# Performance work log

Measured on AMD Instinct MI355X. Metric: run time of the kernel, lower is better.

## Reference

```python
import jax, jax.numpy as jnp
import numpy as np

N_ORDER = 64
PRED_LEN = 720
SEQ_LEN = 720
ENC_IN = 321
BATCH = 16


def _hippo_legs(N):
    # HiPPO-LegS continuous transition (A, B), float64 numpy
    q = np.arange(N, dtype=np.float64)
    col, row = np.meshgrid(q, q)
    r = 2.0 * q + 1.0
    M = -(np.where(row >= col, r, 0.0) - np.diag(q))
    T = np.sqrt(np.diag(2.0 * q + 1.0))
    A = T @ M @ np.linalg.inv(T)
    B = np.diag(T)[:, None].copy()
    return A, B


def _discretize_bilinear(A, B, dt):
    # scipy.signal.cont2discrete(..., method='bilinear') equivalent
    N = A.shape[0]
    I = np.eye(N)
    BL = np.linalg.inv(I - (dt / 2.0) * A)
    Ad = BL @ (I + (dt / 2.0) * A)
    Bd = (BL @ (dt * B)).squeeze(-1)
    return Ad, Bd


def _legendre_eval_matrix(N, dt):
    # ss.eval_legendre(np.arange(N)[:,None], 1 - 2*vals).T via 3-term recurrence
    vals = np.arange(0.0, 1.0, dt)
    x = 1.0 - 2.0 * vals
    Ps = [np.ones_like(x), x]
    for n in range(1, N - 1):
        Ps.append(((2.0 * n + 1.0) * x * Ps[-1] - n * Ps[-2]) / (n + 1.0))
    return np.stack(Ps[:N], axis=0).T  # [len(vals), N]


def setup_inputs() -> dict:
    key = jax.random.key(0)
    k1, k2, k3 = jax.random.split(key, 3)
    dt = 1.0 / PRED_LEN
    A, B = _hippo_legs(N_ORDER)
    Ad, Bd = _discretize_bilinear(A, B, dt)
    eval_matrix = _legendre_eval_matrix(N_ORDER, dt)
    bound = 1.0 / np.sqrt(N_ORDER)  # torch nn.Linear default init range
    return {
        "x_enc": jax.random.normal(k1, (BATCH, SEQ_LEN, ENC_IN), dtype=jnp.float32),
        "A": jnp.asarray(Ad, dtype=jnp.float32),
        "B_vec": jnp.asarray(Bd, dtype=jnp.float32),
        "eval_matrix": jnp.asarray(eval_matrix, dtype=jnp.float32),
        "W_mlp": jax.random.uniform(k2, (N_ORDER, N_ORDER), jnp.float32, -bound, bound),
        "b_mlp": jax.random.uniform(k3, (N_ORDER,), jnp.float32, -bound, bound),
        "affine_weight": jnp.ones((1, 1, ENC_IN), jnp.float32),
        "affine_bias": jnp.zeros((1, 1, ENC_IN), jnp.float32),
    }


def reference(x_enc, A, B_vec, eval_matrix, W_mlp, b_mlp, affine_weight, affine_bias):
    P, N = eval_matrix.shape  # pred_len, proj_degree

    # RevIN-style instance normalization (means/stdev detached in torch)
    means = jax.lax.stop_gradient(jnp.mean(x_enc, axis=1, keepdims=True))
    x = x_enc - means
    stdev = jax.lax.stop_gradient(jnp.sqrt(jnp.var(x, axis=1, keepdims=True) + 1e-5))
    x = x / stdev
    x = x * affine_weight + affine_bias

    x_in = x[:, -P:]                         # [B, P, E]
    xs = jnp.transpose(x_in, (1, 0, 2))      # [P, B, E]: time-major for scan
    c0 = jnp.zeros((x_in.shape[0], x_in.shape[2], N), x_enc.dtype)

    def step(c, f):
        # c_t = c_{t-1} @ A^T + f_t B  (HiPPO-LegS linear recurrence)
        c_new = c @ A.T + f[..., None] * B_vec
        return c_new, c_new

    _, cs = jax.lax.scan(step, c0, xs)       # [P, B, E, N]

    out1 = cs @ W_mlp.T + b_mlp              # mlp over coefficient dim N
    x_dec_c = out1[P - 1]                    # [B, E, N] (seq_len >= pred_len branch)
    x_dec = x_dec_c @ eval_matrix.T          # [B, E, P] Legendre reconstruction
    x_dec = jnp.transpose(x_dec, (0, 2, 1))  # [B, P, E]

    # de-normalize
    x_dec = (x_dec - affine_bias) / (affine_weight + 1e-10)
    x_dec = x_dec * stdev + means
    return x_dec
```

## Files before the change

### kernel.cpp

```cpp
#include <hip/hip_runtime.h>
#include <math.h>

#define BATCH 16
#define SEQ   720
#define ENC   321
#define NORD  64
#define PRED  720
#define NPAIR (BATCH*ENC)

#define WS_KT    0
#define WS_EWT   (WS_KT + PRED*NORD)
#define WS_EVB   (WS_EWT + NORD*PRED)
#define WS_A16   (WS_EVB + PRED)
#define WS_KSUMP (WS_A16 + 4096)
#define WS_G     (WS_KSUMP + 17*64)
#define WS_PSUM  (WS_G + 4*96*4096)
#define WS_PSS   (WS_PSUM + 4*16*6*64)

#define MV4(AR, SVP, OUTV) do {                                                   \
    float _a0=0.f,_a1=0.f,_a2=0.f,_a3=0.f;                                        \
    _Pragma("unroll")                                                             \
    for (int _k = 0; _k < 4; _k++) {                                              \
        float4 _v0 = *(const float4*)&(SVP)[16*_k];                               \
        float4 _v1 = *(const float4*)&(SVP)[16*_k+4];                             \
        float4 _v2 = *(const float4*)&(SVP)[16*_k+8];                             \
        float4 _v3 = *(const float4*)&(SVP)[16*_k+12];                            \
        _a0 += (AR)[16*_k+0]*_v0.x + (AR)[16*_k+1]*_v0.y                          \
             + (AR)[16*_k+2]*_v0.z + (AR)[16*_k+3]*_v0.w;                         \
        _a1 += (AR)[16*_k+4]*_v1.x + (AR)[16*_k+5]*_v1.y                          \
             + (AR)[16*_k+6]*_v1.z + (AR)[16*_k+7]*_v1.w;                         \
        _a2 += (AR)[16*_k+8]*_v2.x + (AR)[16*_k+9]*_v2.y                          \
             + (AR)[16*_k+10]*_v2.z + (AR)[16*_k+11]*_v2.w;                       \
        _a3 += (AR)[16*_k+12]*_v3.x + (AR)[16*_k+13]*_v3.y                        \
             + (AR)[16*_k+14]*_v3.z + (AR)[16*_k+15]*_v3.w;                       \
    }                                                                             \
    OUTV = (_a0+_a1)+(_a2+_a3);                                                   \
} while (0)

__global__ __launch_bounds__(256, 1) void prep(const float* __restrict__ A,
        const float* __restrict__ Bv, float* __restrict__ ws)
{
    __shared__ float sv[4][64];
    const int tid  = threadIdx.x;
    const int lane = tid & 63;
    const int wv   = tid >> 6;
    if (blockIdx.x < 16) {
        float ar[64];
        #pragma unroll
        for (int k = 0; k < 16; k++) {
            float4 v = *(const float4*)&A[lane*64 + 4*k];
            ar[4*k]=v.x; ar[4*k+1]=v.y; ar[4*k+2]=v.z; ar[4*k+3]=v.w;
        }
        const int j = blockIdx.x*4 + wv;
        sv[wv][lane] = (lane == j) ? 1.f : 0.f;
        for (int s = 0; s < 16; s++) {
            float nv;
            MV4(ar, &sv[wv][0], nv);
            sv[wv][lane] = nv;
        }
        ws[WS_A16 + lane*64 + j] = sv[wv][lane];
    } else {
        if (tid >= 64) return;
        float ar[64];
        #pragma unroll
        for (int k = 0; k < 16; k++) {
            float4 v = *(const float4*)&A[lane*64 + 4*k];
            ar[4*k]=v.x; ar[4*k+1]=v.y; ar[4*k+2]=v.z; ar[4*k+3]=v.w;
        }
        float* Kt = ws + WS_KT;
        float bv = Bv[lane];
        sv[0][lane] = bv;
        Kt[(size_t)719*64 + lane] = bv;
        float ksml = bv;
        for (int j = 1; j <= 15; j++) {
            float nv;
            MV4(ar, &sv[0][0], nv);
            sv[0][lane] = nv;
            Kt[(size_t)(719 - j)*64 + lane] = nv;
            ksml += nv;
        }
        ws[WS_KSUMP + 16*64 + lane] = ksml;
    }
}

__global__ __launch_bounds__(256, 1) void chainsEW(const float* __restrict__ evalm,
        const float* __restrict__ W, const float* __restrict__ bm,
        float* __restrict__ ws)
{
    __shared__ float dsm[64*61];
    const int tid  = threadIdx.x;
    const int lane = tid & 63;
    const int wv   = tid >> 6;
    if (blockIdx.x < 16) {
        if (tid >= 64) return;
        float* sv = dsm;
        const int r = blockIdx.x;
        const float* A16 = ws + WS_A16;
        float* Kt = ws + WS_KT;
        float ar16[64];
        #pragma unroll
        for (int k = 0; k < 16; k++) {
            float4 v = *(const float4*)&A16[lane*64 + 4*k];
            ar16[4*k]=v.x; ar16[4*k+1]=v.y; ar16[4*k+2]=v.z; ar16[4*k+3]=v.w;
        }
        float ksml = 0.f;
        sv[lane] = Kt[(size_t)(719 - r)*64 + lane];
        for (int j = r + 16; j <= 719; j += 16) {
            float nv;
            MV4(ar16, sv, nv);
            sv[lane] = nv;
            Kt[(size_t)(719 - j)*64 + lane] = nv;
            ksml += nv;
        }
        ws[WS_KSUMP + r*64 + lane] = ksml;
    } else {
        float* Et = dsm;
        const int r = blockIdx.x - 16;
        float wcol[64];
        #pragma unroll
        for (int n = 0; n < 64; n++) wcol[n] = W[n*64 + lane];
        float bv = bm[lane];
        #pragma unroll
        for (int k = 0; k < 15; k++) {
            int row = wv + k*4;
            int tp = r*60 + row;
            const float* ev = evalm + (size_t)tp*64;
            float a0=0.f,a1=0.f,a2=0.f,a3=0.f;
            #pragma unroll
            for (int kk = 0; kk < 4; kk++) {
                float4 e0_ = *(const float4*)&ev[16*kk];
                float4 e1_ = *(const float4*)&ev[16*kk+4];
                float4 e2_ = *(const float4*)&ev[16*kk+8];
                float4 e3_ = *(const float4*)&ev[16*kk+12];
                a0 += e0_.x*wcol[16*kk+0] + e0_.y*wcol[16*kk+1]
                    + e0_.z*wcol[16*kk+2] + e0_.w*wcol[16*kk+3];
                a1 += e1_.x*wcol[16*kk+4] + e1_.y*wcol[16*kk+5]
                    + e1_.z*wcol[16*kk+6] + e1_.w*wcol[16*kk+7];
                a2 += e2_.x*wcol[16*kk+8] + e2_.y*wcol[16*kk+9]
                    + e2_.z*wcol[16*kk+10] + e2_.w*wcol[16*kk+11];
                a3 += e3_.x*wcol[16*kk+12] + e3_.y*wcol[16*kk+13]
                    + e3_.z*wcol[16*kk+14] + e3_.w*wcol[16*kk+15];
            }
            Et[lane*61 + row] = (a0+a1)+(a2+a3);
            float pv = ev[lane] * bv;
            #pragma unroll
            for (int o = 32; o > 0; o >>= 1) pv += __shfl_down(pv, o);
            if (lane == 0) ws[WS_EVB + tp] = pv;
        }
        __syncthreads();
        for (int idx = tid; idx < 4096; idx += 256) {
            int m = idx >> 6, row = idx & 63;
            if (row < 60)
                ws[WS_EWT + (size_t)m*720 + r*60 + row] = Et[m*61 + row];
        }
    }
}

__device__ inline float4 ldx(const float* __restrict__ x, int b, int t, int e4)
{
    float4 r = make_float4(0.f,0.f,0.f,0.f);
    const float* p = x + ((size_t)b*SEQ + t)*ENC;
    if (e4 + 3 < ENC) r = *(const float4*)&p[e4];
    else {
        if (e4   < ENC) r.x = p[e4];
        if (e4+1 < ENC) r.y = p[e4+1];
        if (e4+2 < ENC) r.z = p[e4+2];
    }
    return r;
}

__global__ __launch_bounds__(256) void k2(const float* __restrict__ x,
        float* __restrict__ ws)
{
    __shared__ float xt[2][12*64];
    __shared__ float ks[2][12*64];
    __shared__ float redn[12*64];
    __shared__ float reds[12*64];
    const int tid = threadIdx.x;
    const int bid = blockIdx.x;
    const int b = bid / 24, rem = bid % 24;
    const int et = rem / 4, tsp = rem % 4;
    const int e0 = et*64, t0 = tsp*180;

    const bool xon = tid < 192;
    const bool kon = tid >= 64;
    const int sx_t  = tid >> 4;
    const int sx_e4 = (tid & 15) * 4;
    const int sk    = tid - 64;
    const int sk_t  = sk >> 4;
    const int sk_m4 = (sk & 15) * 4;

    const float* Kt = ws + WS_KT;
    float s0=0,s1=0,s2=0,s3=0, q0=0,q1=0,q2=0,q3=0;
    float4 rx = make_float4(0,0,0,0), rk = make_float4(0,0,0,0);

    if (xon) rx = ldx(x, b, t0 + sx_t, e0 + sx_e4);
    if (kon) rk = *(const float4*)&Kt[(size_t)(t0 + sk_t)*64 + sk_m4];
    if (xon) {
        *(float4*)&xt[0][sx_t*64 + sx_e4] = rx;
        s0+=rx.x; s1+=rx.y; s2+=rx.z; s3+=rx.w;
        q0+=rx.x*rx.x; q1+=rx.y*rx.y; q2+=rx.z*rx.z; q3+=rx.w*rx.w;
    }
    if (kon) *(float4*)&ks[0][sk_t*64 + sk_m4] = rk;

    const bool con = tid < 128;
    const int elg = tid & 7;
    const int mgr = tid >> 3;
    float acc[8][4];
    #pragma unroll
    for (int j = 0; j < 8; j++)
        #pragma unroll
        for (int i = 0; i < 4; i++) acc[j][i] = 0.f;

    for (int ch = 0; ch < 15; ch++) {
        if (ch + 1 < 15) {
            if (xon) rx = ldx(x, b, t0 + (ch+1)*12 + sx_t, e0 + sx_e4);
            if (kon) rk = *(const float4*)&Kt[(size_t)(t0 + (ch+1)*12 + sk_t)*64 + sk_m4];
        }
        __syncthreads();
        const float* xb = xt[ch & 1];
        const float* kb = ks[ch & 1];
        if (con) {
            #pragma unroll
            for (int tt = 0; tt < 12; tt++) {
                float4 fa = *(const float4*)&xb[tt*64 + elg*8];
                float4 fb = *(const float4*)&xb[tt*64 + elg*8 + 4];
                float4 kv = *(const float4*)&kb[tt*64 + mgr*4];
                acc[0][0]+=fa.x*kv.x; acc[0][1]+=fa.x*kv.y; acc[0][2]+=fa.x*kv.z; acc[0][3]+=fa.x*kv.w;
                acc[1][0]+=fa.y*kv.x; acc[1][1]+=fa.y*kv.y; acc[1][2]+=fa.y*kv.z; acc[1][3]+=fa.y*kv.w;
                acc[2][0]+=fa.z*kv.x; acc[2][1]+=fa.z*kv.y; acc[2][2]+=fa.z*kv.z; acc[2][3]+=fa.z*kv.w;
                acc[3][0]+=fa.w*kv.x; acc[3][1]+=fa.w*kv.y; acc[3][2]+=fa.w*kv.z; acc[3][3]+=fa.w*kv.w;
                acc[4][0]+=fb.x*kv.x; acc[4][1]+=fb.x*kv.y; acc[4][2]+=fb.x*kv.z; acc[4][3]+=fb.x*kv.w;
                acc[5][0]+=fb.y*kv.x; acc[5][1]+=fb.y*kv.y; acc[5][2]+=fb.y*kv.z; acc[5][3]+=fb.y*kv.w;
                acc[6][0]+=fb.z*kv.x; acc[6][1]+=fb.z*kv.y; acc[6][2]+=fb.z*kv.z; acc[6][3]+=fb.z*kv.w;
                acc[7][0]+=fb.w*kv.x; acc[7][1]+=fb.w*kv.y; acc[7][2]+=fb.w*kv.z; acc[7][3]+=fb.w*kv.w;
            }
        }
        if (ch + 1 < 15) {
            if (xon) {
                *(float4*)&xt[(ch+1)&1][sx_t*64 + sx_e4] = rx;
                s0+=rx.x; s1+=rx.y; s2+=rx.z; s3+=rx.w;
                q0+=rx.x*rx.x; q1+=rx.y*rx.y; q2+=rx.z*rx.z; q3+=rx.w*rx.w;
            }
            if (kon) *(float4*)&ks[(ch+1)&1][sk_t*64 + sk_m4] = rk;
        }
    }

    if (con) {
        float* g = ws + WS_G + (size_t)(tsp*96 + b*6 + et)*4096;
        #pragma unroll
        for (int i = 0; i < 4; i++) {
            float* gr = g + (mgr*4 + i)*64 + elg*8;
            *(float4*)&gr[0] = make_float4(acc[0][i], acc[1][i], acc[2][i], acc[3][i]);
            *(float4*)&gr[4] = make_float4(acc[4][i], acc[5][i], acc[6][i], acc[7][i]);
        }
    }

    __syncthreads();
    if (xon) {
        redn[sx_t*64 + sx_e4+0] = s0; redn[sx_t*64 + sx_e4+1] = s1;
        redn[sx_t*64 + sx_e4+2] = s2; redn[sx_t*64 + sx_e4+3] = s3;
        reds[sx_t*64 + sx_e4+0] = q0; reds[sx_t*64 + sx_e4+1] = q1;
        reds[sx_t*64 + sx_e4+2] = q2; reds[sx_t*64 + sx_e4+3] = q3;
    }
    __syncthreads();
    if (tid < 64) {
        float s = 0.f, q = 0.f;
        #pragma unroll
        for (int rr = 0; rr < 12; rr++) { s += redn[rr*64 + tid]; q += reds[rr*64 + tid]; }
        const size_t o = (size_t)((tsp*16 + b)*6 + et)*64 + tid;
        ws[WS_PSUM + o] = s;
        ws[WS_PSS  + o] = q;
    }
}

__global__ __launch_bounds__(256) void k3f(const float* __restrict__ aw,
        const float* __restrict__ ab, const float* __restrict__ ws,
        float* __restrict__ out)
{
    __shared__ float Cm[64*132];
    __shared__ float EWm[64*68];
    __shared__ float ssc[128], ssh[128], smean[128], ssd[128], siaw[128], sabe[128];
    __shared__ float kss[64];
    const int tid = threadIdx.x;
    const int b   = blockIdx.x / 12;
    const int rr  = blockIdx.x % 12;
    const int eT  = rr / 4;
    const int tq  = rr % 4;
    const int e0  = eT * 128;
    const int et0 = eT * 2;

    if (tid < 128) {
        const int el = tid, e = e0 + el;
        const int et = et0 + (el >> 6), eli = el & 63;
        float s = 0.f, q = 0.f;
        #pragma unroll
        for (int tsp = 0; tsp < 4; tsp++) {
            const size_t o = (size_t)((tsp*16 + b)*6 + et)*64 + eli;
            s += ws[WS_PSUM + o];
            q += ws[WS_PSS  + o];
        }
        float mean = s * (1.0f/SEQ);
        float var  = q * (1.0f/SEQ) - mean*mean;
        float sd   = sqrtf(var + 1e-5f);
        if (e < ENC) {
            float a = aw[e], av = ab[e];
            float sc = a / sd;
            ssc[el] = sc; ssh[el] = av - mean*sc;
            smean[el] = mean; ssd[el] = sd;
            siaw[el] = 1.0f/(a + 1e-10f); sabe[el] = av;
        } else {
            ssc[el]=0.f; ssh[el]=0.f; smean[el]=0.f; ssd[el]=0.f; siaw[el]=0.f; sabe[el]=0.f;
        }
    }
    if (tid < 64) {
        float s = 0.f;
        #pragma unroll
        for (int p = 0; p < 17; p++) s += ws[WS_KSUMP + p*64 + tid];
        kss[tid] = s;
    }
    __syncthreads();

    const float* G = ws + WS_G;
    #pragma unroll
    for (int k = 0; k < 8; k++) {
        int slot = k*256 + tid;
        int m = slot >> 5, el4 = (slot & 31) * 4;
        int et = et0 + (el4 >> 6), eli4 = el4 & 63;
        size_t base = (size_t)(b*6 + et)*4096 + m*64 + eli4;
        float4 g0 = *(const float4*)&G[base];
        float4 g1 = *(const float4*)&G[base + (size_t) 96*4096];
        float4 g2 = *(const float4*)&G[base + (size_t)192*4096];
        float4 g3 = *(const float4*)&G[base + (size_t)288*4096];
        float km = kss[m];
        float4 sc = *(const float4*)&ssc[el4];
        float4 sh = *(const float4*)&ssh[el4];
        float4 c;
        c.x = sc.x*(g0.x+g1.x+g2.x+g3.x) + sh.x*km;
        c.y = sc.y*(g0.y+g1.y+g2.y+g3.y) + sh.y*km;
        c.z = sc.z*(g0.z+g1.z+g2.z+g3.z) + sh.z*km;
        c.w = sc.w*(g0.w+g1.w+g2.w+g3.w) + sh.w*km;
        *(float4*)&Cm[m*132 + el4] = c;
    }
    __syncthreads();

    const float* EWT = ws + WS_EWT;
    const float* evb = ws + WS_EVB;
    const int tx = tid & 31;
    const int ty = tid >> 5;

    const int elb = tx*4;
    const int ebase = e0 + elb;
    float4 sab  = *(const float4*)&sabe[elb];
    float4 sia  = *(const float4*)&siaw[elb];
    float4 ssd4 = *(const float4*)&ssd[elb];
    float4 smn  = *(const float4*)&smean[elb];

    for (int ti = 0; ti < 3; ti++) {
        const int tt0 = (tq*3 + ti) * 64;
        if (ti > 0) __syncthreads();
        #pragma unroll
        for (int k = 0; k < 4; k++) {
            int slot = k*256 + tid;
            int m = slot >> 4, t4 = (slot & 15)*4;
            int tp = tt0 + t4;
            float4 v;
            if (tp + 3 < PRED) v = *(const float4*)&EWT[(size_t)m*720 + tp];
            else {
                v = make_float4(0.f,0.f,0.f,0.f);
                if (tp   < PRED) v.x = EWT[(size_t)m*720 + tp];
                if (tp+1 < PRED) v.y = EWT[(size_t)m*720 + tp+1];
                if (tp+2 < PRED) v.z = EWT[(size_t)m*720 + tp+2];
            }
            *(float4*)&EWm[m*68 + t4] = v;
        }
        __syncthreads();

        float acc[8][4];
        #pragma unroll
        for (int i = 0; i < 8; i++)
            #pragma unroll
            for (int j = 0; j < 4; j++) acc[i][j] = 0.f;

        #pragma unroll 4
        for (int m = 0; m < 64; m++) {
            float4 c4 = *(const float4*)&Cm[m*132 + tx*4];
            float4 w0 = *(const float4*)&EWm[m*68 + ty*8];
            float4 w1 = *(const float4*)&EWm[m*68 + ty*8 + 4];
            acc[0][0]+=w0.x*c4.x; acc[0][1]+=w0.x*c4.y; acc[0][2]+=w0.x*c4.z; acc[0][3]+=w0.x*c4.w;
            acc[1][0]+=w0.y*c4.x; acc[1][1]+=w0.y*c4.y; acc[1][2]+=w0.y*c4.z; acc[1][3]+=w0.y*c4.w;
            acc[2][0]+=w0.z*c4.x; acc[2][1]+=w0.z*c4.y; acc[2][2]+=w0.z*c4.z; acc[2][3]+=w0.z*c4.w;
            acc[3][0]+=w0.w*c4.x; acc[3][1]+=w0.w*c4.y; acc[3][2]+=w0.w*c4.z; acc[3][3]+=w0.w*c4.w;
            acc[4][0]+=w1.x*c4.x; acc[4][1]+=w1.x*c4.y; acc[4][2]+=w1.x*c4.z; acc[4][3]+=w1.x*c4.w;
            acc[5][0]+=w1.y*c4.x; acc[5][1]+=w1.y*c4.y; acc[5][2]+=w1.y*c4.z; acc[5][3]+=w1.y*c4.w;
            acc[6][0]+=w1.z*c4.x; acc[6][1]+=w1.z*c4.y; acc[6][2]+=w1.z*c4.z; acc[6][3]+=w1.z*c4.w;
            acc[7][0]+=w1.w*c4.x; acc[7][1]+=w1.w*c4.y; acc[7][2]+=w1.w*c4.z; acc[7][3]+=w1.w*c4.w;
        }

        #pragma unroll
        for (int i = 0; i < 8; i++) {
            int tp = tt0 + ty*8 + i;
            if (tp < PRED) {
                float ev = evb[tp];
                float* op = out + ((size_t)b*PRED + tp)*ENC;
                if (ebase + 3 < ENC) {
                    float4 o;
                    o.x = (acc[i][0] + ev - sab.x) * sia.x * ssd4.x + smn.x;
                    o.y = (acc[i][1] + ev - sab.y) * sia.y * ssd4.y + smn.y;
                    o.z = (acc[i][2] + ev - sab.z) * sia.z * ssd4.z + smn.z;
                    o.w = (acc[i][3] + ev - sab.w) * sia.w * ssd4.w + smn.w;
                    *(float4*)&op[ebase] = o;
                } else {
                    if (ebase   < ENC) op[ebase  ] = (acc[i][0]+ev-sab.x)*sia.x*ssd4.x+smn.x;
                    if (ebase+1 < ENC) op[ebase+1] = (acc[i][1]+ev-sab.y)*sia.y*ssd4.y+smn.y;
                    if (ebase+2 < ENC) op[ebase+2] = (acc[i][2]+ev-sab.z)*sia.z*ssd4.z+smn.z;
                }
            }
        }
    }
}

extern "C" void kernel_launch(void* const* d_in, const int* in_sizes, int n_in,
                              void* d_out, int out_size, void* d_ws, size_t ws_size,
                              hipStream_t stream)
{
    const float* x     = (const float*)d_in[0];
    const float* A     = (const float*)d_in[1];
    const float* Bv    = (const float*)d_in[2];
    const float* evalm = (const float*)d_in[3];
    const float* W     = (const float*)d_in[4];
    const float* bm    = (const float*)d_in[5];
    const float* aw    = (const float*)d_in[6];
    const float* ab    = (const float*)d_in[7];
    float* ws  = (float*)d_ws;
    float* out = (float*)d_out;

    prep    <<<17, 256, 0, stream>>>(A, Bv, ws);
    chainsEW<<<28, 256, 0, stream>>>(evalm, W, bm, ws);
    k2      <<<BATCH*6*4, 256, 0, stream>>>(x, ws);
    k3f     <<<192, 256, 0, stream>>>(aw, ab, ws, out);
}
```

Measured before the change: 151.4 us.

## Restructure k2 as register-direct slab reduction and retile k3f output GEMM

k2 drops its shared-memory double-buffered tiles and has each thread stream x and the kernel rows straight from global memory into register accumulators. The time axis is split into 8 slabs instead of 4, doubling the grid. k3f now loads the whole 192-step EW tile once and computes a 12x8 register tile per thread, and the denormalisation is folded into a single multiply-add. The changes aim for more parallelism and fewer barriers, at the cost of more partial sums to reduce and more uncoalesced-like strided x loads.

```diff
diff --git a/kernel.cpp b/kernel.cpp
--- a/kernel.cpp
+++ b/kernel.cpp
@@ -6,7 +6,9 @@
 #define ENC   321
 #define NORD  64
 #define PRED  720
-#define NPAIR (BATCH*ENC)
+
+#define NSLAB 8
+#define TSLAB 90
 
 #define WS_KT    0
 #define WS_EWT   (WS_KT + PRED*NORD)
@@ -14,8 +16,8 @@
 #define WS_A16   (WS_EVB + PRED)
 #define WS_KSUMP (WS_A16 + 4096)
 #define WS_G     (WS_KSUMP + 17*64)
-#define WS_PSUM  (WS_G + 4*96*4096)
-#define WS_PSS   (WS_PSUM + 4*16*6*64)
+#define WS_PSUM  (WS_G + NSLAB*96*4096)
+#define WS_PSS   (WS_PSUM + NSLAB*16*6*64)
 
 #define MV4(AR, SVP, OUTV) do {                                                   \
     float _a0=0.f,_a1=0.f,_a2=0.f,_a3=0.f;                                        \
@@ -156,137 +158,81 @@
     }
 }
 
-__device__ inline float4 ldx(const float* __restrict__ x, int b, int t, int e4)
-{
-    float4 r = make_float4(0.f,0.f,0.f,0.f);
-    const float* p = x + ((size_t)b*SEQ + t)*ENC;
-    if (e4 + 3 < ENC) r = *(const float4*)&p[e4];
-    else {
-        if (e4   < ENC) r.x = p[e4];
-        if (e4+1 < ENC) r.y = p[e4+1];
-        if (e4+2 < ENC) r.z = p[e4+2];
-    }
-    return r;
-}
-
 __global__ __launch_bounds__(256) void k2(const float* __restrict__ x,
         float* __restrict__ ws)
 {
-    __shared__ float xt[2][12*64];
-    __shared__ float ks[2][12*64];
-    __shared__ float redn[12*64];
-    __shared__ float reds[12*64];
     const int tid = threadIdx.x;
     const int bid = blockIdx.x;
-    const int b = bid / 24, rem = bid % 24;
-    const int et = rem / 4, tsp = rem % 4;
-    const int e0 = et*64, t0 = tsp*180;
-
-    const bool xon = tid < 192;
-    const bool kon = tid >= 64;
-    const int sx_t  = tid >> 4;
-    const int sx_e4 = (tid & 15) * 4;
-    const int sk    = tid - 64;
-    const int sk_t  = sk >> 4;
-    const int sk_m4 = (sk & 15) * 4;
-
-    const float* Kt = ws + WS_KT;
-    float s0=0,s1=0,s2=0,s3=0, q0=0,q1=0,q2=0,q3=0;
-    float4 rx = make_float4(0,0,0,0), rk = make_float4(0,0,0,0);
-
-    if (xon) rx = ldx(x, b, t0 + sx_t, e0 + sx_e4);
-    if (kon) rk = *(const float4*)&Kt[(size_t)(t0 + sk_t)*64 + sk_m4];
-    if (xon) {
-        *(float4*)&xt[0][sx_t*64 + sx_e4] = rx;
-        s0+=rx.x; s1+=rx.y; s2+=rx.z; s3+=rx.w;
-        q0+=rx.x*rx.x; q1+=rx.y*rx.y; q2+=rx.z*rx.z; q3+=rx.w*rx.w;
-    }
-    if (kon) *(float4*)&ks[0][sk_t*64 + sk_m4] = rk;
-
-    const bool con = tid < 128;
-    const int elg = tid & 7;
-    const int mgr = tid >> 3;
-    float acc[8][4];
-    #pragma unroll
-    for (int j = 0; j < 8; j++)
-        #pragma unroll
-        for (int i = 0; i < 4; i++) acc[j][i] = 0.f;
-
-    for (int ch = 0; ch < 15; ch++) {
-        if (ch + 1 < 15) {
-            if (xon) rx = ldx(x, b, t0 + (ch+1)*12 + sx_t, e0 + sx_e4);
-            if (kon) rk = *(const float4*)&Kt[(size_t)(t0 + (ch+1)*12 + sk_t)*64 + sk_m4];
-        }
-        __syncthreads();
-        const float* xb = xt[ch & 1];
-        const float* kb = ks[ch & 1];
-        if (con) {
-            #pragma unroll
-            for (int tt = 0; tt < 12; tt++) {
-                float4 fa = *(const float4*)&xb[tt*64 + elg*8];
-                float4 fb = *(const float4*)&xb[tt*64 + elg*8 + 4];
-                float4 kv = *(const float4*)&kb[tt*64 + mgr*4];
-                acc[0][0]+=fa.x*kv.x; acc[0][1]+=fa.x*kv.y; acc[0][2]+=fa.x*kv.z; acc[0][3]+=fa.x*kv.w;
-                acc[1][0]+=fa.y*kv.x; acc[1][1]+=fa.y*kv.y; acc[1][2]+=fa.y*kv.z; acc[1][3]+=fa.y*kv.w;
-                acc[2][0]+=fa.z*kv.x; acc[2][1]+=fa.z*kv.y; acc[2][2]+=fa.z*kv.z; acc[2][3]+=fa.z*kv.w;
-                acc[3][0]+=fa.w*kv.x; acc[3][1]+=fa.w*kv.y; acc[3][2]+=fa.w*kv.z; acc[3][3]+=fa.w*kv.w;
-                acc[4][0]+=fb.x*kv.x; acc[4][1]+=fb.x*kv.y; acc[4][2]+=fb.x*kv.z; acc[4][3]+=fb.x*kv.w;
-                acc[5][0]+=fb.y*kv.x; acc[5][1]+=fb.y*kv.y; acc[5][2]+=fb.y*kv.z; acc[5][3]+=fb.y*kv.w;
-                acc[6][0]+=fb.z*kv.x; acc[6][1]+=fb.z*kv.y; acc[6][2]+=fb.z*kv.z; acc[6][3]+=fb.z*kv.w;
-                acc[7][0]+=fb.w*kv.x; acc[7][1]+=fb.w*kv.y; acc[7][2]+=fb.w*kv.z; acc[7][3]+=fb.w*kv.w;
-            }
-        }
-        if (ch + 1 < 15) {
-            if (xon) {
-                *(float4*)&xt[(ch+1)&1][sx_t*64 + sx_e4] = rx;
-                s0+=rx.x; s1+=rx.y; s2+=rx.z; s3+=rx.w;
-                q0+=rx.x*rx.x; q1+=rx.y*rx.y; q2+=rx.z*rx.z; q3+=rx.w*rx.w;
-            }
-            if (kon) *(float4*)&ks[(ch+1)&1][sk_t*64 + sk_m4] = rk;
-        }
-    }
-
-    if (con) {
-        float* g = ws + WS_G + (size_t)(tsp*96 + b*6 + et)*4096;
-        #pragma unroll
-        for (int i = 0; i < 4; i++) {
-            float* gr = g + (mgr*4 + i)*64 + elg*8;
-            *(float4*)&gr[0] = make_float4(acc[0][i], acc[1][i], acc[2][i], acc[3][i]);
-            *(float4*)&gr[4] = make_float4(acc[4][i], acc[5][i], acc[6][i], acc[7][i]);
-        }
-    }
-
-    __syncthreads();
-    if (xon) {
-        redn[sx_t*64 + sx_e4+0] = s0; redn[sx_t*64 + sx_e4+1] = s1;
-        redn[sx_t*64 + sx_e4+2] = s2; redn[sx_t*64 + sx_e4+3] = s3;
-        reds[sx_t*64 + sx_e4+0] = q0; reds[sx_t*64 + sx_e4+1] = q1;
-        reds[sx_t*64 + sx_e4+2] = q2; reds[sx_t*64 + sx_e4+3] = q3;
-    }
-    __syncthreads();
-    if (tid < 64) {
-        float s = 0.f, q = 0.f;
-        #pragma unroll
-        for (int rr = 0; rr < 12; rr++) { s += redn[rr*64 + tid]; q += reds[rr*64 + tid]; }
-        const size_t o = (size_t)((tsp*16 + b)*6 + et)*64 + tid;
-        ws[WS_PSUM + o] = s;
-        ws[WS_PSS  + o] = q;
-    }
-}
+    const int b = bid / 48, rem = bid % 48;
+    const int et = rem >> 3, tsp = rem & 7;
+    const int e0 = et*64, t0 = tsp*TSLAB;
+
+    const int lane = tid & 63;
+    const int wv   = tid >> 6;
+    const int eg   = lane & 7;
+    const int mg   = lane >> 3;
+    const int el   = wv*16 + eg*2;
+    const int e    = e0 + el;
+
+    const float* xp = x + ((size_t)b*SEQ + t0)*ENC + e;
+    const float* kp = ws + WS_KT + (size_t)t0*64 + mg*8;
+
+    float a0[8], a1[8];
+    #pragma unroll
+    for (int i = 0; i < 8; i++) { a0[i]=0.f; a1[i]=0.f; }
+    float s0=0.f, s1=0.f, q0=0.f, q1=0.f;
+    const bool v1 = (e + 1 < ENC);
+    const bool v0 = (e < ENC);
+
+    #pragma unroll 6
+    for (int t = 0; t < TSLAB; t++) {
+        float xa = 0.f, xb = 0.f;
+        if (v1)      { float2 xv = *(const float2*)xp; xa = xv.x; xb = xv.y; }
+        else if (v0) { xa = *xp; }
+        float4 k0 = *(const float4*)kp;
+        float4 k1 = *(const float4*)(kp + 4);
+        a0[0]+=k0.x*xa; a1[0]+=k0.x*xb;
+        a0[1]+=k0.y*xa; a1[1]+=k0.y*xb;
+        a0[2]+=k0.z*xa; a1[2]+=k0.z*xb;
+        a0[3]+=k0.w*xa; a1[3]+=k0.w*xb;
+        a0[4]+=k1.x*xa; a1[4]+=k1.x*xb;
+        a0[5]+=k1.y*xa; a1[5]+=k1.y*xb;
+        a0[6]+=k1.z*xa; a1[6]+=k1.z*xb;
+        a0[7]+=k1.w*xa; a1[7]+=k1.w*xb;
+        s0 += xa; q0 += xa*xa;
+        s1 += xb; q1 += xb*xb;
+        xp += ENC; kp += 64;
+    }
+
+    float* g = ws + WS_G + (size_t)(tsp*96 + b*6 + et)*4096 + el;
+    #pragma unroll
+    for (int i = 0; i < 8; i++)
+        *(float2*)&g[(mg*8 + i)*64] = make_float2(a0[i], a1[i]);
+
+    if (mg == 0) {
+        const size_t o = (size_t)((tsp*16 + b)*6 + et)*64 + el;
+        *(float2*)&ws[WS_PSUM + o] = make_float2(s0, s1);
+        *(float2*)&ws[WS_PSS  + o] = make_float2(q0, q1);
+    }
+}
+
+#define K3ROW(r, wvv) \
+    acc[r][0]+=(wvv)*c0.x; acc[r][1]+=(wvv)*c0.y; acc[r][2]+=(wvv)*c0.z; acc[r][3]+=(wvv)*c0.w; \
+    acc[r][4]+=(wvv)*c1.x; acc[r][5]+=(wvv)*c1.y; acc[r][6]+=(wvv)*c1.z; acc[r][7]+=(wvv)*c1.w;
 
 __global__ __launch_bounds__(256) void k3f(const float* __restrict__ aw,
         const float* __restrict__ ab, const float* __restrict__ ws,
         float* __restrict__ out)
 {
-    __shared__ float Cm[64*132];
-    __shared__ float EWm[64*68];
-    __shared__ float ssc[128], ssh[128], smean[128], ssd[128], siaw[128], sabe[128];
+    __shared__ float Cm[64*192];
+    __shared__ float EWm[64*196];
+    __shared__ float ssc[128], ssh[128], sP[128], sQ[128];
     __shared__ float kss[64];
     const int tid = threadIdx.x;
     const int b   = blockIdx.x / 12;
     const int rr  = blockIdx.x % 12;
-    const int eT  = rr / 4;
-    const int tq  = rr % 4;
+    const int eT  = rr >> 2;
+    const int tq  = rr & 3;
     const int e0  = eT * 128;
     const int et0 = eT * 2;
 
@@ -295,7 +241,7 @@
         const int et = et0 + (el >> 6), eli = el & 63;
         float s = 0.f, q = 0.f;
         #pragma unroll
-        for (int tsp = 0; tsp < 4; tsp++) {
+        for (int tsp = 0; tsp < NSLAB; tsp++) {
             const size_t o = (size_t)((tsp*16 + b)*6 + et)*64 + eli;
             s += ws[WS_PSUM + o];
             q += ws[WS_PSS  + o];
@@ -306,11 +252,11 @@
         if (e < ENC) {
             float a = aw[e], av = ab[e];
             float sc = a / sd;
+            float P  = sd / (a + 1e-10f);
             ssc[el] = sc; ssh[el] = av - mean*sc;
-            smean[el] = mean; ssd[el] = sd;
-            siaw[el] = 1.0f/(a + 1e-10f); sabe[el] = av;
+            sP[el]  = P;  sQ[el]  = mean - av*P;
         } else {
-            ssc[el]=0.f; ssh[el]=0.f; smean[el]=0.f; ssd[el]=0.f; siaw[el]=0.f; sabe[el]=0.f;
+            ssc[el]=0.f; ssh[el]=0.f; sP[el]=0.f; sQ[el]=0.f;
         }
     }
     if (tid < 64) {
@@ -328,93 +274,97 @@
         int m = slot >> 5, el4 = (slot & 31) * 4;
         int et = et0 + (el4 >> 6), eli4 = el4 & 63;
         size_t base = (size_t)(b*6 + et)*4096 + m*64 + eli4;
-        float4 g0 = *(const float4*)&G[base];
-        float4 g1 = *(const float4*)&G[base + (size_t) 96*4096];
-        float4 g2 = *(const float4*)&G[base + (size_t)192*4096];
-        float4 g3 = *(const float4*)&G[base + (size_t)288*4096];
+        float4 gs = make_float4(0.f,0.f,0.f,0.f);
+        #pragma unroll
+        for (int s2 = 0; s2 < NSLAB; s2++) {
+            float4 gv = *(const float4*)&G[base + (size_t)s2*96*4096];
+            gs.x += gv.x; gs.y += gv.y; gs.z += gv.z; gs.w += gv.w;
+        }
         float km = kss[m];
         float4 sc = *(const float4*)&ssc[el4];
         float4 sh = *(const float4*)&ssh[el4];
         float4 c;
-        c.x = sc.x*(g0.x+g1.x+g2.x+g3.x) + sh.x*km;
-        c.y = sc.y*(g0.y+g1.y+g2.y+g3.y) + sh.y*km;
-        c.z = sc.z*(g0.z+g1.z+g2.z+g3.z) + sh.z*km;
-        c.w = sc.w*(g0.w+g1.w+g2.w+g3.w) + sh.w*km;
-        *(float4*)&Cm[m*132 + el4] = c;
+        c.x = sc.x*gs.x + sh.x*km;
+        c.y = sc.y*gs.y + sh.y*km;
+        c.z = sc.z*gs.z + sh.z*km;
+        c.w = sc.w*gs.w + sh.w*km;
+        *(float4*)&Cm[m*192 + (el4>>3)*12 + (el4&7)] = c;
+    }
+
+    const float* EWT = ws + WS_EWT;
+    #pragma unroll
+    for (int it = 0; it < 12; it++) {
+        int slot = it*256 + tid;
+        int m = slot / 48, t4 = (slot % 48) * 4;
+        int tp = tq*192 + t4;
+        float4 v;
+        if (tp + 3 < PRED) v = *(const float4*)&EWT[(size_t)m*720 + tp];
+        else {
+            v = make_float4(0.f,0.f,0.f,0.f);
+            if (tp   < PRED) v.x = EWT[(size_t)m*720 + tp];
+            if (tp+1 < PRED) v.y = EWT[(size_t)m*720 + tp+1];
+            if (tp+2 < PRED) v.z = EWT[(size_t)m*720 + tp+2];
+        }
+        *(float4*)&EWm[m*196 + t4] = v;
     }
     __syncthreads();
 
-    const float* EWT = ws + WS_EWT;
+    const int tx = tid & 15;
+    const int ty = tid >> 4;
+    float acc[12][8];
+    #pragma unroll
+    for (int r = 0; r < 12; r++)
+        #pragma unroll
+        for (int j = 0; j < 8; j++) acc[r][j] = 0.f;
+
+    const float* cb = Cm  + tx*12;
+    const float* wb = EWm + ty*12;
+    #pragma unroll 2
+    for (int m = 0; m < 64; m++) {
+        float4 c0 = *(const float4*)&cb[m*192];
+        float4 c1 = *(const float4*)&cb[m*192 + 4];
+        float4 w0 = *(const float4*)&wb[m*196];
+        float4 w1 = *(const float4*)&wb[m*196 + 4];
+        float4 w2 = *(const float4*)&wb[m*196 + 8];
+        K3ROW(0,  w0.x) K3ROW(1,  w0.y) K3ROW(2,  w0.z) K3ROW(3,  w0.w)
+        K3ROW(4,  w1.x) K3ROW(5,  w1.y) K3ROW(6,  w1.z) K3ROW(7,  w1.w)
+        K3ROW(8,  w2.x) K3ROW(9,  w2.y) K3ROW(10, w2.z) K3ROW(11, w2.w)
+    }
+
+    const int elb = tx*8;
+    const int eb  = e0 + elb;
+    float4 Pa = *(const float4*)&sP[elb];
+    float4 Pb = *(const float4*)&sP[elb+4];
+    float4 Qa = *(const float4*)&sQ[elb];
+    float4 Qb = *(const float4*)&sQ[elb+4];
     const float* evb = ws + WS_EVB;
-    const int tx = tid & 31;
-    const int ty = tid >> 5;
-
-    const int elb = tx*4;
-    const int ebase = e0 + elb;
-    float4 sab  = *(const float4*)&sabe[elb];
-    float4 sia  = *(const float4*)&siaw[elb];
-    float4 ssd4 = *(const float4*)&ssd[elb];
-    float4 smn  = *(const float4*)&smean[elb];
-
-    for (int ti = 0; ti < 3; ti++) {
-        const int tt0 = (tq*3 + ti) * 64;
-        if (ti > 0) __syncthreads();
-        #pragma unroll
-        for (int k = 0; k < 4; k++) {
-            int slot = k*256 + tid;
-            int m = slot >> 4, t4 = (slot & 15)*4;
-            int tp = tt0 + t4;
-            float4 v;
-            if (tp + 3 < PRED) v = *(const float4*)&EWT[(size_t)m*720 + tp];
-            else {
-                v = make_float4(0.f,0.f,0.f,0.f);
-                if (tp   < PRED) v.x = EWT[(size_t)m*720 + tp];
-                if (tp+1 < PRED) v.y = EWT[(size_t)m*720 + tp+1];
-                if (tp+2 < PRED) v.z = EWT[(size_t)m*720 + tp+2];
-            }
-            *(float4*)&EWm[m*68 + t4] = v;
-        }
-        __syncthreads();
-
-        float acc[8][4];
-        #pragma unroll
-        for (int i = 0; i < 8; i++)
-            #pragma unroll
-            for (int j = 0; j < 4; j++) acc[i][j] = 0.f;
-
-        #pragma unroll 4
-        for (int m = 0; m < 64; m++) {
-            float4 c4 = *(const float4*)&Cm[m*132 + tx*4];
-            float4 w0 = *(const float4*)&EWm[m*68 + ty*8];
-            float4 w1 = *(const float4*)&EWm[m*68 + ty*8 + 4];
-            acc[0][0]+=w0.x*c4.x; acc[0][1]+=w0.x*c4.y; acc[0][2]+=w0.x*c4.z; acc[0][3]+=w0.x*c4.w;
-            acc[1][0]+=w0.y*c4.x; acc[1][1]+=w0.y*c4.y; acc[1][2]+=w0.y*c4.z; acc[1][3]+=w0.y*c4.w;
-            acc[2][0]+=w0.z*c4.x; acc[2][1]+=w0.z*c4.y; acc[2][2]+=w0.z*c4.z; acc[2][3]+=w0.z*c4.w;
-            acc[3][0]+=w0.w*c4.x; acc[3][1]+=w0.w*c4.y; acc[3][2]+=w0.w*c4.z; acc[3][3]+=w0.w*c4.w;
-            acc[4][0]+=w1.x*c4.x; acc[4][1]+=w1.x*c4.y; acc[4][2]+=w1.x*c4.z; acc[4][3]+=w1.x*c4.w;
-            acc[5][0]+=w1.y*c4.x; acc[5][1]+=w1.y*c4.y; acc[5][2]+=w1.y*c4.z; acc[5][3]+=w1.y*c4.w;
-            acc[6][0]+=w1.z*c4.x; acc[6][1]+=w1.z*c4.y; acc[6][2]+=w1.z*c4.z; acc[6][3]+=w1.z*c4.w;
-            acc[7][0]+=w1.w*c4.x; acc[7][1]+=w1.w*c4.y; acc[7][2]+=w1.w*c4.z; acc[7][3]+=w1.w*c4.w;
-        }
-
-        #pragma unroll
-        for (int i = 0; i < 8; i++) {
-            int tp = tt0 + ty*8 + i;
-            if (tp < PRED) {
-                float ev = evb[tp];
-                float* op = out + ((size_t)b*PRED + tp)*ENC;
-                if (ebase + 3 < ENC) {
-                    float4 o;
-                    o.x = (acc[i][0] + ev - sab.x) * sia.x * ssd4.x + smn.x;
-                    o.y = (acc[i][1] + ev - sab.y) * sia.y * ssd4.y + smn.y;
-                    o.z = (acc[i][2] + ev - sab.z) * sia.z * ssd4.z + smn.z;
-                    o.w = (acc[i][3] + ev - sab.w) * sia.w * ssd4.w + smn.w;
-                    *(float4*)&op[ebase] = o;
-                } else {
-                    if (ebase   < ENC) op[ebase  ] = (acc[i][0]+ev-sab.x)*sia.x*ssd4.x+smn.x;
-                    if (ebase+1 < ENC) op[ebase+1] = (acc[i][1]+ev-sab.y)*sia.y*ssd4.y+smn.y;
-                    if (ebase+2 < ENC) op[ebase+2] = (acc[i][2]+ev-sab.z)*sia.z*ssd4.z+smn.z;
-                }
+    #pragma unroll
+    for (int r = 0; r < 12; r++) {
+        int tp = tq*192 + ty*12 + r;
+        if (tp < PRED) {
+            float ev = evb[tp];
+            float* op = out + ((size_t)b*PRED + tp)*ENC;
+            if (eb + 7 < ENC) {
+                float4 o0, o1;
+                o0.x = (acc[r][0]+ev)*Pa.x + Qa.x;
+                o0.y = (acc[r][1]+ev)*Pa.y + Qa.y;
+                o0.z = (acc[r][2]+ev)*Pa.z + Qa.z;
+                o0.w = (acc[r][3]+ev)*Pa.w + Qa.w;
+                o1.x = (acc[r][4]+ev)*Pb.x + Qb.x;
+                o1.y = (acc[r][5]+ev)*Pb.y + Qb.y;
+                o1.z = (acc[r][6]+ev)*Pb.z + Qb.z;
+                o1.w = (acc[r][7]+ev)*Pb.w + Qb.w;
+                *(float4*)&op[eb]   = o0;
+                *(float4*)&op[eb+4] = o1;
+            } else {
+                if (eb   < ENC) op[eb  ] = (acc[r][0]+ev)*Pa.x + Qa.x;
+                if (eb+1 < ENC) op[eb+1] = (acc[r][1]+ev)*Pa.y + Qa.y;
+                if (eb+2 < ENC) op[eb+2] = (acc[r][2]+ev)*Pa.z + Qa.z;
+                if (eb+3 < ENC) op[eb+3] = (acc[r][3]+ev)*Pa.w + Qa.w;
+                if (eb+4 < ENC) op[eb+4] = (acc[r][4]+ev)*Pb.x + Qb.x;
+                if (eb+5 < ENC) op[eb+5] = (acc[r][5]+ev)*Pb.y + Qb.y;
+                if (eb+6 < ENC) op[eb+6] = (acc[r][6]+ev)*Pb.z + Qb.z;
+                if (eb+7 < ENC) op[eb+7] = (acc[r][7]+ev)*Pb.w + Qb.w;
             }
         }
     }
@@ -437,6 +387,6 @@
 
     prep    <<<17, 256, 0, stream>>>(A, Bv, ws);
     chainsEW<<<28, 256, 0, stream>>>(evalm, W, bm, ws);
-    k2      <<<BATCH*6*4, 256, 0, stream>>>(x, ws);
+    k2      <<<16*6*NSLAB, 256, 0, stream>>>(x, ws);
     k3f     <<<192, 256, 0, stream>>>(aw, ab, ws, out);
 }
```

Measured after the change: 157.5 us. +4.0%, slower.

## Enlarge k3f register tile to 12x8 and load full EW slice once

Applied to the files above, without the earlier changes.

The output-projection kernel now loads its whole 192-step slice of the evaluation weights into shared memory once, instead of three 64-step passes each with its own barrier. Each thread computes a 12x8 register tile instead of 8x4, which raises FMA-to-LDS ratio, and the C tile uses a padded 12-stride layout. The de-normalization is folded into one multiply-add per element. In exchange it uses more shared memory (about 100KB) and more registers, which may reduce occupancy.

```diff
diff --git a/kernel.cpp b/kernel.cpp
--- a/kernel.cpp
+++ b/kernel.cpp
@@ -274,19 +274,23 @@
     }
 }
 
+#define K3ROW(r, wvv) \
+    acc[r][0]+=(wvv)*c0.x; acc[r][1]+=(wvv)*c0.y; acc[r][2]+=(wvv)*c0.z; acc[r][3]+=(wvv)*c0.w; \
+    acc[r][4]+=(wvv)*c1.x; acc[r][5]+=(wvv)*c1.y; acc[r][6]+=(wvv)*c1.z; acc[r][7]+=(wvv)*c1.w;
+
 __global__ __launch_bounds__(256) void k3f(const float* __restrict__ aw,
         const float* __restrict__ ab, const float* __restrict__ ws,
         float* __restrict__ out)
 {
-    __shared__ float Cm[64*132];
-    __shared__ float EWm[64*68];
-    __shared__ float ssc[128], ssh[128], smean[128], ssd[128], siaw[128], sabe[128];
+    __shared__ float Cm[64*192];
+    __shared__ float EWm[64*196];
+    __shared__ float ssc[128], ssh[128], sP[128], sQ[128];
     __shared__ float kss[64];
     const int tid = threadIdx.x;
     const int b   = blockIdx.x / 12;
     const int rr  = blockIdx.x % 12;
-    const int eT  = rr / 4;
-    const int tq  = rr % 4;
+    const int eT  = rr >> 2;
+    const int tq  = rr & 3;
     const int e0  = eT * 128;
     const int et0 = eT * 2;
 
@@ -306,11 +310,11 @@
         if (e < ENC) {
             float a = aw[e], av = ab[e];
             float sc = a / sd;
+            float P  = sd / (a + 1e-10f);
             ssc[el] = sc; ssh[el] = av - mean*sc;
-            smean[el] = mean; ssd[el] = sd;
-            siaw[el] = 1.0f/(a + 1e-10f); sabe[el] = av;
+            sP[el]  = P;  sQ[el]  = mean - av*P;
         } else {
-            ssc[el]=0.f; ssh[el]=0.f; smean[el]=0.f; ssd[el]=0.f; siaw[el]=0.f; sabe[el]=0.f;
+            ssc[el]=0.f; ssh[el]=0.f; sP[el]=0.f; sQ[el]=0.f;
         }
     }
     if (tid < 64) {
@@ -340,81 +344,83 @@
         c.y = sc.y*(g0.y+g1.y+g2.y+g3.y) + sh.y*km;
         c.z = sc.z*(g0.z+g1.z+g2.z+g3.z) + sh.z*km;
         c.w = sc.w*(g0.w+g1.w+g2.w+g3.w) + sh.w*km;
-        *(float4*)&Cm[m*132 + el4] = c;
+        *(float4*)&Cm[m*192 + (el4>>3)*12 + (el4&7)] = c;
+    }
+
+    const float* EWT = ws + WS_EWT;
+    #pragma unroll
+    for (int it = 0; it < 12; it++) {
+        int slot = it*256 + tid;
+        int m = slot / 48, t4 = (slot % 48) * 4;
+        int tp = tq*192 + t4;
+        float4 v;
+        if (tp + 3 < PRED) v = *(const float4*)&EWT[(size_t)m*720 + tp];
+        else {
+            v = make_float4(0.f,0.f,0.f,0.f);
+            if (tp   < PRED) v.x = EWT[(size_t)m*720 + tp];
+            if (tp+1 < PRED) v.y = EWT[(size_t)m*720 + tp+1];
+            if (tp+2 < PRED) v.z = EWT[(size_t)m*720 + tp+2];
+        }
+        *(float4*)&EWm[m*196 + t4] = v;
     }
     __syncthreads();
 
-    const float* EWT = ws + WS_EWT;
+    const int tx = tid & 15;
+    const int ty = tid >> 4;
+    float acc[12][8];
+    #pragma unroll
+    for (int r = 0; r < 12; r++)
+        #pragma unroll
+        for (int j = 0; j < 8; j++) acc[r][j] = 0.f;
+
+    const float* cb = Cm  + tx*12;
+    const float* wb = EWm + ty*12;
+    #pragma unroll 2
+    for (int m = 0; m < 64; m++) {
+        float4 c0 = *(const float4*)&cb[m*192];
+        float4 c1 = *(const float4*)&cb[m*192 + 4];
+        float4 w0 = *(const float4*)&wb[m*196];
+        float4 w1 = *(const float4*)&wb[m*196 + 4];
+        float4 w2 = *(const float4*)&wb[m*196 + 8];
+        K3ROW(0,  w0.x) K3ROW(1,  w0.y) K3ROW(2,  w0.z) K3ROW(3,  w0.w)
+        K3ROW(4,  w1.x) K3ROW(5,  w1.y) K3ROW(6,  w1.z) K3ROW(7,  w1.w)
+        K3ROW(8,  w2.x) K3ROW(9,  w2.y) K3ROW(10, w2.z) K3ROW(11, w2.w)
+    }
+
+    const int elb = tx*8;
+    const int eb  = e0 + elb;
+    float4 Pa = *(const float4*)&sP[elb];
+    float4 Pb = *(const float4*)&sP[elb+4];
+    float4 Qa = *(const float4*)&sQ[elb];
+    float4 Qb = *(const float4*)&sQ[elb+4];
     const float* evb = ws + WS_EVB;
-    const int tx = tid & 31;
-    const int ty = tid >> 5;
-
-    const int elb = tx*4;
-    const int ebase = e0 + elb;
-    float4 sab  = *(const float4*)&sabe[elb];
-    float4 sia  = *(const float4*)&siaw[elb];
-    float4 ssd4 = *(const float4*)&ssd[elb];
-    float4 smn  = *(const float4*)&smean[elb];
-
-    for (int ti = 0; ti < 3; ti++) {
-        const int tt0 = (tq*3 + ti) * 64;
-        if (ti > 0) __syncthreads();
-        #pragma unroll
-        for (int k = 0; k < 4; k++) {
-            int slot = k*256 + tid;
-            int m = slot >> 4, t4 = (slot & 15)*4;
-            int tp = tt0 + t4;
-            float4 v;
-            if (tp + 3 < PRED) v = *(const float4*)&EWT[(size_t)m*720 + tp];
-            else {
-                v = make_float4(0.f,0.f,0.f,0.f);
-                if (tp   < PRED) v.x = EWT[(size_t)m*720 + tp];
-                if (tp+1 < PRED) v.y = EWT[(size_t)m*720 + tp+1];
-                if (tp+2 < PRED) v.z = EWT[(size_t)m*720 + tp+2];
-            }
-            *(float4*)&EWm[m*68 + t4] = v;
-        }
-        __syncthreads();
-
-        float acc[8][4];
-        #pragma unroll
-        for (int i = 0; i < 8; i++)
-            #pragma unroll
-            for (int j = 0; j < 4; j++) acc[i][j] = 0.f;
-
-        #pragma unroll 4
-        for (int m = 0; m < 64; m++) {
-            float4 c4 = *(const float4*)&Cm[m*132 + tx*4];
-            float4 w0 = *(const float4*)&EWm[m*68 + ty*8];
-            float4 w1 = *(const float4*)&EWm[m*68 + ty*8 + 4];
-            acc[0][0]+=w0.x*c4.x; acc[0][1]+=w0.x*c4.y; acc[0][2]+=w0.x*c4.z; acc[0][3]+=w0.x*c4.w;
-            acc[1][0]+=w0.y*c4.x; acc[1][1]+=w0.y*c4.y; acc[1][2]+=w0.y*c4.z; acc[1][3]+=w0.y*c4.w;
-            acc[2][0]+=w0.z*c4.x; acc[2][1]+=w0.z*c4.y; acc[2][2]+=w0.z*c4.z; acc[2][3]+=w0.z*c4.w;
-            acc[3][0]+=w0.w*c4.x; acc[3][1]+=w0.w*c4.y; acc[3][2]+=w0.w*c4.z; acc[3][3]+=w0.w*c4.w;
-            acc[4][0]+=w1.x*c4.x; acc[4][1]+=w1.x*c4.y; acc[4][2]+=w1.x*c4.z; acc[4][3]+=w1.x*c4.w;
-            acc[5][0]+=w1.y*c4.x; acc[5][1]+=w1.y*c4.y; acc[5][2]+=w1.y*c4.z; acc[5][3]+=w1.y*c4.w;
-            acc[6][0]+=w1.z*c4.x; acc[6][1]+=w1.z*c4.y; acc[6][2]+=w1.z*c4.z; acc[6][3]+=w1.z*c4.w;
-            acc[7][0]+=w1.w*c4.x; acc[7][1]+=w1.w*c4.y; acc[7][2]+=w1.w*c4.z; acc[7][3]+=w1.w*c4.w;
-        }
-
-        #pragma unroll
-        for (int i = 0; i < 8; i++) {
-            int tp = tt0 + ty*8 + i;
-            if (tp < PRED) {
-                float ev = evb[tp];
-                float* op = out + ((size_t)b*PRED + tp)*ENC;
-                if (ebase + 3 < ENC) {
-                    float4 o;
-                    o.x = (acc[i][0] + ev - sab.x) * sia.x * ssd4.x + smn.x;
-                    o.y = (acc[i][1] + ev - sab.y) * sia.y * ssd4.y + smn.y;
-                    o.z = (acc[i][2] + ev - sab.z) * sia.z * ssd4.z + smn.z;
-                    o.w = (acc[i][3] + ev - sab.w) * sia.w * ssd4.w + smn.w;
-                    *(float4*)&op[ebase] = o;
-                } else {
-                    if (ebase   < ENC) op[ebase  ] = (acc[i][0]+ev-sab.x)*sia.x*ssd4.x+smn.x;
-                    if (ebase+1 < ENC) op[ebase+1] = (acc[i][1]+ev-sab.y)*sia.y*ssd4.y+smn.y;
-                    if (ebase+2 < ENC) op[ebase+2] = (acc[i][2]+ev-sab.z)*sia.z*ssd4.z+smn.z;
-                }
+    #pragma unroll
+    for (int r = 0; r < 12; r++) {
+        int tp = tq*192 + ty*12 + r;
+        if (tp < PRED) {
+            float ev = evb[tp];
+            float* op = out + ((size_t)b*PRED + tp)*ENC;
+            if (eb + 7 < ENC) {
+                float4 o0, o1;
+                o0.x = (acc[r][0]+ev)*Pa.x + Qa.x;
+                o0.y = (acc[r][1]+ev)*Pa.y + Qa.y;
+                o0.z = (acc[r][2]+ev)*Pa.z + Qa.z;
+                o0.w = (acc[r][3]+ev)*Pa.w + Qa.w;
+                o1.x = (acc[r][4]+ev)*Pb.x + Qb.x;
+                o1.y = (acc[r][5]+ev)*Pb.y + Qb.y;
+                o1.z = (acc[r][6]+ev)*Pb.z + Qb.z;
+                o1.w = (acc[r][7]+ev)*Pb.w + Qb.w;
+                *(float4*)&op[eb]   = o0;
+                *(float4*)&op[eb+4] = o1;
+            } else {
+                if (eb   < ENC) op[eb  ] = (acc[r][0]+ev)*Pa.x + Qa.x;
+                if (eb+1 < ENC) op[eb+1] = (acc[r][1]+ev)*Pa.y + Qa.y;
+                if (eb+2 < ENC) op[eb+2] = (acc[r][2]+ev)*Pa.z + Qa.z;
+                if (eb+3 < ENC) op[eb+3] = (acc[r][3]+ev)*Pa.w + Qa.w;
+                if (eb+4 < ENC) op[eb+4] = (acc[r][4]+ev)*Pb.x + Qb.x;
+                if (eb+5 < ENC) op[eb+5] = (acc[r][5]+ev)*Pb.y + Qb.y;
+                if (eb+6 < ENC) op[eb+6] = (acc[r][6]+ev)*Pb.z + Qb.z;
+                if (eb+7 < ENC) op[eb+7] = (acc[r][7]+ev)*Pb.w + Qb.w;
             }
         }
     }
```

After: 148.9 us. About the same (-1.7%).
